# Kernel optimization log

Measured on AMD Instinct MI355X. Metric: run time of the kernel, lower is better.

The kernel has to match this reference:

```python
import jax, jax.numpy as jnp
import numpy as np

B, NA, LAT, HID, AF, L = 512, 58, 64, 128, 10, 2
N = B * NA
E = N * 16


def silu(x):
    return x * jax.nn.sigmoid(x)


def setup_inputs() -> dict:
    key = jax.random.key(0)
    ks = list(jax.random.split(key, 32))

    def p(k, shape, fan_in):
        return jax.random.normal(k, shape, jnp.float32) / np.sqrt(fan_in)

    inp = {
        "z": jax.random.normal(ks[0], (B, LAT), jnp.float32),
        "atom_types": jax.random.uniform(ks[1], (N, AF), jnp.float32),
        "edge_index": jax.random.randint(ks[2], (2, E), 0, N, jnp.int64),
        "init_coords": jax.random.normal(ks[3], (NA, 3), jnp.float32) * 0.1,
        "latent_w": p(ks[4], (LAT, HID), LAT), "latent_b": jnp.zeros((HID,), jnp.float32),
        "atom_w": p(ks[5], (AF, HID), AF), "atom_b": jnp.zeros((HID,), jnp.float32),
        # per-layer stacked params (leading dim = num_layers)
        "edge_w1": p(ks[6], (L, 2 * HID + 1, HID), 2 * HID + 1), "edge_b1": jnp.zeros((L, HID), jnp.float32),
        "edge_w2": p(ks[7], (L, HID, HID), HID), "edge_b2": jnp.zeros((L, HID), jnp.float32),
        "node_w1": p(ks[8], (L, 2 * HID, HID), 2 * HID), "node_b1": jnp.zeros((L, HID), jnp.float32),
        "node_w2": p(ks[9], (L, HID, HID), HID), "node_b2": jnp.zeros((L, HID), jnp.float32),
        "coord_w1": p(ks[10], (L, HID, HID), HID), "coord_b1": jnp.zeros((L, HID), jnp.float32),
        "coord_w2": p(ks[11], (L, HID, 1), HID),  # no bias
        "ln_g": jnp.ones((L, HID), jnp.float32), "ln_b": jnp.zeros((L, HID), jnp.float32),
        "head_w1": p(ks[12], (HID, HID // 2), HID), "head_b1": jnp.zeros((HID // 2,), jnp.float32),
        "head_w2": p(ks[13], (HID // 2, 3), HID // 2), "head_b2": jnp.zeros((3,), jnp.float32),
    }
    return inp


def _layer(h, pos, row, col, ew1, eb1, ew2, eb2, nw1, nb1, nw2, nb2, cw1, cb1, cw2, lg, lb):
    n = h.shape[0]
    xi, xj = h[row], h[col]                      # [E,HID] gathers
    rel = pos[row] - pos[col]                    # [E,3]
    d2 = jnp.clip(jnp.sum(rel * rel, axis=-1, keepdims=True), 1e-6, 1e6)
    ef = jnp.concatenate([xi, xj, d2], axis=-1)  # [E,2H+1]
    m = silu(silu(ef @ ew1 + eb1) @ ew2 + eb2)   # edge MLP messages [E,HID]
    agg = jax.ops.segment_sum(m, row, num_segments=n)
    hn = silu(jnp.concatenate([h, agg], axis=-1) @ nw1 + nb1) @ nw2 + nb2
    mu = jnp.mean(hn, axis=-1, keepdims=True)
    var = jnp.mean((hn - mu) ** 2, axis=-1, keepdims=True)
    hn = (hn - mu) * jax.lax.rsqrt(var + 1e-5) * lg + lb
    cw = jnp.clip(silu(m @ cw1 + cb1) @ cw2, -1.0, 1.0)  # [E,1]
    upd = jax.ops.segment_sum(cw * rel, row, num_segments=n)  # [N,3]
    deg = jax.ops.segment_sum(jnp.ones((row.shape[0],), pos.dtype), row, num_segments=n)[:, None]
    pos_new = pos + upd / (deg + 1e-6)
    return hn, pos_new


def reference(z, atom_types, edge_index, init_coords, latent_w, latent_b, atom_w, atom_b,
              edge_w1, edge_b1, edge_w2, edge_b2, node_w1, node_b1, node_w2, node_b2,
              coord_w1, coord_b1, coord_w2, ln_g, ln_b, head_w1, head_b1, head_w2, head_b2):
    b = z.shape[0]
    na = init_coords.shape[0]
    n = b * na
    h = z @ latent_w + latent_b                              # [B,HID]
    h = jnp.broadcast_to(h[:, None, :], (b, na, h.shape[-1])).reshape(n, -1)
    h = h + (atom_types @ atom_w + atom_b)
    pos = jnp.broadcast_to(init_coords[None], (b, na, 3)).reshape(n, 3)
    row, col = edge_index[0], edge_index[1]
    for l in range(edge_w1.shape[0]):
        h, pos = _layer(h, pos, row, col,
                        edge_w1[l], edge_b1[l], edge_w2[l], edge_b2[l],
                        node_w1[l], node_b1[l], node_w2[l], node_b2[l],
                        coord_w1[l], coord_b1[l], coord_w2[l], ln_g[l], ln_b[l])
    delta = silu(h @ head_w1 + head_b1) @ head_w2 + head_b2
    return pos + delta
```

## Files before the change

### kernel.cpp

```cpp
#include <hip/hip_runtime.h>
#include <hip/hip_bf16.h>

#define BB 512
#define NA 58
#define LAT 64
#define HID 128
#define AF 10
#define NL 2
#define NN (BB*NA)
#define NE (NN*16)
#define ET 64
#define NTILE (NE/ET)
#define PBLK 768

typedef __attribute__((ext_vector_type(8))) short s8;
typedef __attribute__((ext_vector_type(4))) float f4;

struct CvtDesc {
    const void* src[24];
    float*      dst[24];
    int         len[24];
};

struct PackJobs {
    const float* src[11];
    short*       dst[11];
    int          K[11];
    int          mode[11];
};

__device__ __forceinline__ float siluf(float x) {
    return x * __builtin_amdgcn_rcpf(1.0f + __expf(-x));
}

__device__ __forceinline__ short f2b(float x) {
    __hip_bfloat16 b = __float2bfloat16(x);
    return *(short*)&b;
}

__device__ __forceinline__ float b2f(short s) {
    return __uint_as_float(((unsigned int)(unsigned short)s) << 16);
}

__global__ void k_detect(const unsigned short* __restrict__ z16,
                         const unsigned int* __restrict__ e32,
                         int* __restrict__ flags) {
    __shared__ int sbf, si64;
    if (threadIdx.x == 0) { sbf = 0; si64 = 0; }
    __syncthreads();
    int c1 = 0, c2 = 0;
    for (int i = threadIdx.x; i < 1024; i += 256) {
        unsigned short v = z16[2*i];
        int e = (v >> 7) & 0xFF;
        if (e >= 100 && e <= 140) c1++;
        if (e32[2*i + 1] == 0u) c2++;
    }
    atomicAdd(&sbf, c1);
    atomicAdd(&si64, c2);
    __syncthreads();
    if (threadIdx.x == 0) {
        flags[0] = (sbf  > 600) ? 1 : 0;
        flags[1] = (si64 > 600) ? 1 : 0;
    }
}

__global__ void k_convert(CvtDesc d, const int* __restrict__ flags) {
    int a = blockIdx.y;
    int i = blockIdx.x * blockDim.x + threadIdx.x;
    int n = d.len[a];
    if (i >= n) return;
    if (flags[0]) {
        d.dst[a][i] = __bfloat162float(((const __hip_bfloat16*)d.src[a])[i]);
    } else {
        d.dst[a][i] = ((const float*)d.src[a])[i];
    }
}

__global__ void k_packall(PackJobs pj) {
    int j = blockIdx.y;
    int idx = blockIdx.x * 256 + threadIdx.x;
    const float* w = pj.src[j];
    short* o = pj.dst[j];
    int mode = pj.mode[j];
    if (mode == 0) {
        int K = pj.K[j];
        if (idx >= 128*K) return;
        int jj = idx & 7;
        int l  = (idx >> 3) & 63;
        int rest = idx >> 9;
        int KC = K >> 5;
        int kc = rest % KC;
        int nt = rest / KC;
        int n = nt*16 + (l & 15);
        int k = kc*32 + (l >> 4)*8 + jj;
        o[idx] = f2b(w[k*128 + n]);
    } else if (mode == 1) {
        if (idx >= 32768) return;
        int jj = idx & 7;
        int l  = (idx >> 3) & 63;
        int rest = idx >> 9;
        int kc = rest & 3;
        int nt = rest >> 2;
        int n = nt*16 + (l & 15);
        int k = kc*32 + (l >> 4)*8 + jj;
        float v = (n < 128) ? w[k*128 + n] : w[(128 + k)*128 + (n - 128)];
        o[idx] = f2b(v);
    } else {
        if (idx >= 8192) return;
        int jj = idx & 7;
        int l  = (idx >> 3) & 63;
        int rest = idx >> 9;
        int kc = rest & 3;
        int nt = rest >> 2;
        int n = nt*16 + (l & 15);
        int k = kc*32 + (l >> 4)*8 + jj;
        o[idx] = f2b(w[k*64 + n]);
    }
}

__global__ void k_hist(const int* __restrict__ eidx, const int* __restrict__ flags,
                       int* __restrict__ cnt) {
    int e = blockIdx.x * 256 + threadIdx.x;
    if (e >= NE) return;
    int is64 = flags[1];
    int r = eidx[is64 ? 2*(long)e : (long)e];
    atomicAdd(&cnt[r], 1);
}

__global__ __launch_bounds__(1024) void k_scan(const int* __restrict__ cnt,
                                               int* __restrict__ rowStart,
                                               int* __restrict__ cursor) {
    __shared__ int part[1024];
    int t = threadIdx.x;
    int base = t * 29;
    int loc[29];
    int s = 0;
    #pragma unroll
    for (int i = 0; i < 29; ++i) { loc[i] = s; s += cnt[base + i]; }
    part[t] = s;
    __syncthreads();
    for (int d = 1; d < 1024; d <<= 1) {
        int v = (t >= d) ? part[t - d] : 0;
        __syncthreads();
        part[t] += v;
        __syncthreads();
    }
    int pre = (t == 0) ? 0 : part[t - 1];
    #pragma unroll
    for (int i = 0; i < 29; ++i) {
        int v = pre + loc[i];
        rowStart[base + i] = v;
        cursor[base + i] = v;
    }
    if (t == 1023) rowStart[NN] = pre + s;
}

__global__ void k_scatter(const int* __restrict__ eidx, const int* __restrict__ flags,
                          int* __restrict__ cursor,
                          int* __restrict__ rS, int* __restrict__ cS) {
    int e = blockIdx.x * 256 + threadIdx.x;
    if (e >= NE) return;
    int is64 = flags[1];
    long ge = e, gc = (long)e + NE;
    int r = eidx[is64 ? 2*ge : ge];
    int c = eidx[is64 ? 2*gc : gc];
    int p = atomicAdd(&cursor[r], 1);
    rS[p] = r; cS[p] = c;
}

__global__ __launch_bounds__(256) void k_init3(
    const float* __restrict__ z, const float* __restrict__ lw,
    const float* __restrict__ lbz,
    const float* __restrict__ at,
    const float* __restrict__ aw, const float* __restrict__ ab,
    const float* __restrict__ ic,
    float* __restrict__ pos, short* __restrict__ hb,
    const short* __restrict__ wcat0, const float* __restrict__ b10,
    short* __restrict__ H1, float* __restrict__ agg, float* __restrict__ upd)
{
    __shared__ short x[64][136];
    __shared__ float awS[AF][HID];
    __shared__ float atS[64][AF+2];
    __shared__ float zbS[3][LAT];
    __shared__ float hzS[3][HID];
    const int tid = threadIdx.x;
    const int n0 = blockIdx.x * 64;
    const int b0 = n0 / NA;
    const int nb = (n0 + 63) / NA - b0 + 1;

    for (int i = tid; i < AF*HID; i += 256) awS[i/HID][i%HID] = aw[i];
    for (int i = tid; i < 64*AF; i += 256)
        atS[i/AF][i%AF] = at[(long)(n0 + i/AF)*AF + i%AF];
    for (int i = tid; i < nb*LAT; i += 256) {
        int bi = i / LAT, k = i - bi*LAT;
        int bidx = b0 + bi;
        zbS[bi][k] = (bidx < BB) ? z[bidx*LAT + k] : 0.f;
    }
    __syncthreads();

    for (int i = tid; i < nb*HID; i += 256) {
        int bi = i / HID, c = i - bi*HID;
        float acc = lbz[c];
        #pragma unroll
        for (int k = 0; k < LAT; ++k) acc += zbS[bi][k] * lw[k*HID + c];
        hzS[bi][c] = acc;
    }
    __syncthreads();

    #pragma unroll
    for (int it = 0; it < 32; ++it) {
        int idx = it*256 + tid;
        int r = idx >> 7, c = idx & 127;
        int n = n0 + r;
        float v = hzS[n/NA - b0][c] + ab[c];
        #pragma unroll
        for (int f = 0; f < AF; ++f) v += atS[r][f]*awS[f][c];
        short s = f2b(v);
        x[r][c] = s;
        hb[(long)n*HID + c] = s;
    }
    if (tid < 192) {
        int i = tid/3, d = tid - i*3;
        int n = n0 + i;
        pos[n*3 + d] = ic[(n % NA)*3 + d];
        upd[n*3 + d] = 0.f;
    }
    {
        f4* a4 = (f4*)(agg + (long)n0*HID);
        for (int j = tid; j < 64*HID/4; j += 256) a4[j] = (f4)0.f;
    }
    __syncthreads();

    const int l = tid & 63, w = tid >> 6;
    const int l16 = l & 15, quad = l >> 4;
    f4 acc[4][4];
    #pragma unroll
    for (int mt = 0; mt < 4; ++mt)
        #pragma unroll
        for (int nt4 = 0; nt4 < 4; ++nt4) acc[mt][nt4] = (f4)0.f;
    #pragma unroll
    for (int kc = 0; kc < 4; ++kc) {
        s8 a[4];
        #pragma unroll
        for (int mt = 0; mt < 4; ++mt)
            a[mt] = *(const s8*)&x[mt*16 + l16][kc*32 + quad*8];
        #pragma unroll
        for (int nt4 = 0; nt4 < 4; ++nt4) {
            int nt = w*4 + nt4;
            s8 b = *(const s8*)(wcat0 + (((size_t)nt*4 + kc)*64 + l)*8);
            #pragma unroll
            for (int mt = 0; mt < 4; ++mt)
                acc[mt][nt4] = __builtin_amdgcn_mfma_f32_16x16x32_bf16(a[mt], b, acc[mt][nt4], 0, 0, 0);
        }
    }
    #pragma unroll
    for (int nt4 = 0; nt4 < 4; ++nt4) {
        int col = (w*4 + nt4)*16 + l16;
        float bias = (col < 128) ? b10[col] : 0.f;
        #pragma unroll
        for (int mt = 0; mt < 4; ++mt)
            #pragma unroll
            for (int i = 0; i < 4; ++i) {
                int row = mt*16 + quad*4 + i;
                H1[(long)(n0 + row)*256 + col] = f2b(acc[mt][nt4][i] + bias);
            }
    }
}

__global__ __launch_bounds__(256, 3) void k_edge8(
    const short* __restrict__ H1,
    const int* __restrict__ rS, const int* __restrict__ cS,
    const float* __restrict__ pos,
    const float* __restrict__ w1c,
    const short* __restrict__ w2p, const float* __restrict__ b2,
    const short* __restrict__ c1p, const float* __restrict__ cb1,
    const float* __restrict__ cw2,
    float* __restrict__ agg, float* __restrict__ upd)
{
    __shared__ short t1[2][ET][136];
    __shared__ short mm[ET][136];
    __shared__ int   rIs[2][ET], cIs[2][ET];
    __shared__ float sred[ET];

    const int tid = threadIdx.x;
    const int l = tid & 63, w = tid >> 6;
    const int l16 = l & 15, quad = l >> 4;
    const int c0 = (2*w)*16 + l16, c1c = (2*w+1)*16 + l16;
    const int half = tid >> 7, ch = tid & 127;
    const int q = tid & 15;
    const int esub = tid >> 4;

    float wv[8];
    #pragma unroll
    for (int j = 0; j < 8; ++j) wv[j] = w1c[q*8 + j];

    s8 w2f[8], c1f[8];
    #pragma unroll
    for (int kc = 0; kc < 4; ++kc) {
        w2f[kc]     = *(const s8*)(w2p + (((size_t)(2*w)*4 + kc)*64 + l)*8);
        w2f[4 + kc] = *(const s8*)(w2p + (((size_t)(2*w+1)*4 + kc)*64 + l)*8);
        c1f[kc]     = *(const s8*)(c1p + (((size_t)(2*w)*4 + kc)*64 + l)*8);
        c1f[4 + kc] = *(const s8*)(c1p + (((size_t)(2*w+1)*4 + kc)*64 + l)*8);
    }
    const float bia2_0 = b2[c0],  bia2_1 = b2[c1c];
    const float biac_0 = cb1[c0], biac_1 = cb1[c1c];
    const float cw0    = cw2[c0], cw1v   = cw2[c1c];

    int   pri[4], pci[4];
    float pd2[4];
    auto PREIDX = [&](int T) {
        long eb = (long)T * ET;
        #pragma unroll
        for (int it = 0; it < 4; ++it) {
            int e = esub + 16*it;
            int r = rS[eb + e], c = cS[eb + e];
            pri[it] = r; pci[it] = c;
            float rx = pos[r*3+0] - pos[c*3+0];
            float ry = pos[r*3+1] - pos[c*3+1];
            float rz = pos[r*3+2] - pos[c*3+2];
            pd2[it] = fminf(fmaxf(rx*rx + ry*ry + rz*rz, 1e-6f), 1e6f);
        }
    };

    int T = blockIdx.x;
    PREIDX(T);
    #pragma unroll
    for (int it = 0; it < 4; ++it) {
        s8 va = *(const s8*)(H1 + (long)pri[it]*256 + q*8);
        s8 vb = *(const s8*)(H1 + (long)pci[it]*256 + 128 + q*8);
        float d2 = pd2[it];
        s8 o;
        #pragma unroll
        for (int j = 0; j < 8; ++j)
            o[j] = f2b(siluf(b2f(va[j]) + b2f(vb[j]) + d2*wv[j]));
        *(s8*)&t1[0][esub + 16*it][q*8] = o;
    }
    if (q == 0) {
        #pragma unroll
        for (int it = 0; it < 4; ++it) {
            rIs[0][esub + 16*it] = pri[it];
            cIs[0][esub + 16*it] = pci[it];
        }
    }
    if (tid < ET) sred[tid] = 0.f;
    int Tn = T + PBLK;
    if (Tn < NTILE) PREIDX(Tn);
    __syncthreads();

    int b = 0;
    while (true) {
        const bool hasNext = (Tn < NTILE);

        {
            f4 acc[4][2];
            #pragma unroll
            for (int mt = 0; mt < 4; ++mt) { acc[mt][0] = (f4)0.f; acc[mt][1] = (f4)0.f; }
            #pragma unroll
            for (int it = 0; it < 4; ++it) {
                s8 va, vb;
                if (hasNext) {
                    va = *(const s8*)(H1 + (long)pri[it]*256 + q*8);
                    vb = *(const s8*)(H1 + (long)pci[it]*256 + 128 + q*8);
                }
                #pragma unroll
                for (int mt = 0; mt < 4; ++mt) {
                    s8 a = *(const s8*)&t1[b][mt*16 + l16][it*32 + quad*8];
                    acc[mt][0] = __builtin_amdgcn_mfma_f32_16x16x32_bf16(a, w2f[it],     acc[mt][0], 0, 0, 0);
                    acc[mt][1] = __builtin_amdgcn_mfma_f32_16x16x32_bf16(a, w2f[4 + it], acc[mt][1], 0, 0, 0);
                }
                if (hasNext) {
                    float d2 = pd2[it];
                    s8 o;
                    #pragma unroll
                    for (int j = 0; j < 8; ++j)
                        o[j] = f2b(siluf(b2f(va[j]) + b2f(vb[j]) + d2*wv[j]));
                    *(s8*)&t1[b^1][esub + 16*it][q*8] = o;
                }
            }
            if (hasNext && q == 0) {
                #pragma unroll
                for (int it = 0; it < 4; ++it) {
                    rIs[b^1][esub + 16*it] = pri[it];
                    cIs[b^1][esub + 16*it] = pci[it];
                }
            }
            #pragma unroll
            for (int mt = 0; mt < 4; ++mt) {
                #pragma unroll
                for (int i = 0; i < 4; ++i) {
                    int row = mt*16 + quad*4 + i;
                    mm[row][c0]  = f2b(siluf(acc[mt][0][i] + bia2_0));
                    mm[row][c1c] = f2b(siluf(acc[mt][1][i] + bia2_1));
                }
            }
        }
        __syncthreads();

        {
            int e0 = half * 32;
            int cur = rIs[b][e0];
            float a = 0.f;
            #pragma unroll
            for (int e = e0; e < e0 + 32; ++e) {
                int r = rIs[b][e];
                if (r != cur) {
                    atomicAdd(&agg[(long)cur*HID + ch], a);
                    a = 0.f; cur = r;
                }
                a += b2f(mm[e][ch]);
            }
            atomicAdd(&agg[(long)cur*HID + ch], a);
        }
        {
            f4 acc[4][2];
            #pragma unroll
            for (int mt = 0; mt < 4; ++mt) { acc[mt][0] = (f4)0.f; acc[mt][1] = (f4)0.f; }
            #pragma unroll
            for (int kc = 0; kc < 4; ++kc) {
                #pragma unroll
                for (int mt = 0; mt < 4; ++mt) {
                    s8 a = *(const s8*)&mm[mt*16 + l16][kc*32 + quad*8];
                    acc[mt][0] = __builtin_amdgcn_mfma_f32_16x16x32_bf16(a, c1f[kc],     acc[mt][0], 0, 0, 0);
                    acc[mt][1] = __builtin_amdgcn_mfma_f32_16x16x32_bf16(a, c1f[4 + kc], acc[mt][1], 0, 0, 0);
                }
            }
            #pragma unroll
            for (int mt = 0; mt < 4; ++mt) {
                #pragma unroll
                for (int i = 0; i < 4; ++i) {
                    float p = siluf(acc[mt][0][i] + biac_0) * cw0
                            + siluf(acc[mt][1][i] + biac_1) * cw1v;
                    p += __shfl_xor(p, 1);
                    p += __shfl_xor(p, 2);
                    p += __shfl_xor(p, 4);
                    p += __shfl_xor(p, 8);
                    if (l16 == 0) {
                        int row = mt*16 + quad*4 + i;
                        atomicAdd(&sred[row], p);
                    }
                }
            }
        }
        int Tnn = Tn + PBLK;
        if (hasNext && Tnn < NTILE) PREIDX(Tnn);
        __syncthreads();

        if (tid < ET) {
            float cwv = fminf(fmaxf(sred[tid], -1.f), 1.f);
            sred[tid] = 0.f;
            int r = rIs[b][tid], c = cIs[b][tid];
            float rx = pos[r*3+0] - pos[c*3+0];
            float ry = pos[r*3+1] - pos[c*3+1];
            float rz = pos[r*3+2] - pos[c*3+2];
            atomicAdd(&upd[r*3+0], cwv*rx);
            atomicAdd(&upd[r*3+1], cwv*ry);
            atomicAdd(&upd[r*3+2], cwv*rz);
        }
        if (!hasNext) break;
        T = Tn; Tn = Tnn; b ^= 1;
    }
}

__global__ __launch_bounds__(256) void k_node_mfma(
    short* __restrict__ hb, float* __restrict__ agg,
    const short* __restrict__ w1p, const float* __restrict__ b1n,
    const short* __restrict__ w2p, const float* __restrict__ b2n,
    const float* __restrict__ lg, const float* __restrict__ lb,
    float* __restrict__ pos, float* __restrict__ upd,
    const int* __restrict__ rowStart,
    const short* __restrict__ wcatn, const float* __restrict__ b1next,
    short* __restrict__ H1,
    const short* __restrict__ hw1p, const float* __restrict__ hb1,
    const float* __restrict__ hw2, const float* __restrict__ hb2,
    void* __restrict__ out, const int* __restrict__ flags)
{
    __shared__ short x[64][264];
    __shared__ short t1[64][144];
    __shared__ float mus[64], rstds[64];
    __shared__ float posS[64][3];
    float (*hn)[132] = (float (*)[132])&x[0][0];
    float (*hid)[68] = (float (*)[68])&x[0][0];

    const int tid = threadIdx.x;
    const int n0 = blockIdx.x * 64;

    #pragma unroll
    for (int it = 0; it < 4; ++it) {
        int idx = it*256 + tid;
        int e = idx >> 4, qq = idx & 15;
        *(int4*)&x[e][qq*8] = *(const int4*)(hb + (long)(n0+e)*HID + qq*8);
    }
    #pragma unroll
    for (int it = 0; it < 8; ++it) {
        int idx = it*256 + tid;
        int e = idx >> 5, qq = idx & 31;
        float4 v = *(const float4*)(agg + (long)(n0+e)*HID + qq*4);
        short4 sv;
        sv.x = f2b(v.x); sv.y = f2b(v.y); sv.z = f2b(v.z); sv.w = f2b(v.w);
        *(short4*)&x[e][128 + qq*4] = sv;
    }
    __syncthreads();

    {
        f4* a4 = (f4*)(agg + (long)n0*HID);
        for (int j = tid; j < 64*HID/4; j += 256) a4[j] = (f4)0.f;
    }

    const int l = tid & 63, w = tid >> 6;
    const int l16 = l & 15, quad = l >> 4;
    const int nt0 = 2*w, nt1 = 2*w + 1;
    const int c0 = nt0*16 + l16, c1c = nt1*16 + l16;

    {
        f4 acc[4][2];
        #pragma unroll
        for (int mt = 0; mt < 4; ++mt) { acc[mt][0] = (f4)0.f; acc[mt][1] = (f4)0.f; }
        #pragma unroll
        for (int kc = 0; kc < 8; ++kc) {
            s8 b0  = *(const s8*)(w1p + (((size_t)nt0*8 + kc)*64 + l)*8);
            s8 b1f = *(const s8*)(w1p + (((size_t)nt1*8 + kc)*64 + l)*8);
            #pragma unroll
            for (int mt = 0; mt < 4; ++mt) {
                s8 a = *(const s8*)&x[mt*16 + l16][kc*32 + quad*8];
                acc[mt][0] = __builtin_amdgcn_mfma_f32_16x16x32_bf16(a, b0,  acc[mt][0], 0, 0, 0);
                acc[mt][1] = __builtin_amdgcn_mfma_f32_16x16x32_bf16(a, b1f, acc[mt][1], 0, 0, 0);
            }
        }
        float bia0 = b1n[c0], bia1 = b1n[c1c];
        #pragma unroll
        for (int mt = 0; mt < 4; ++mt) {
            #pragma unroll
            for (int i = 0; i < 4; ++i) {
                int row = mt*16 + quad*4 + i;
                t1[row][c0]  = f2b(siluf(acc[mt][0][i] + bia0));
                t1[row][c1c] = f2b(siluf(acc[mt][1][i] + bia1));
            }
        }
    }
    __syncthreads();

    {
        f4 acc[4][2];
        #pragma unroll
        for (int mt = 0; mt < 4; ++mt) { acc[mt][0] = (f4)0.f; acc[mt][1] = (f4)0.f; }
        #pragma unroll
        for (int kc = 0; kc < 4; ++kc) {
            s8 b0  = *(const s8*)(w2p + (((size_t)nt0*4 + kc)*64 + l)*8);
            s8 b1f = *(const s8*)(w2p + (((size_t)nt1*4 + kc)*64 + l)*8);
            #pragma unroll
            for (int mt = 0; mt < 4; ++mt) {
                s8 a = *(const s8*)&t1[mt*16 + l16][kc*32 + quad*8];
                acc[mt][0] = __builtin_amdgcn_mfma_f32_16x16x32_bf16(a, b0,  acc[mt][0], 0, 0, 0);
                acc[mt][1] = __builtin_amdgcn_mfma_f32_16x16x32_bf16(a, b1f, acc[mt][1], 0, 0, 0);
            }
        }
        float bia0 = b2n[c0], bia1 = b2n[c1c];
        __syncthreads();
        #pragma unroll
        for (int mt = 0; mt < 4; ++mt) {
            #pragma unroll
            for (int i = 0; i < 4; ++i) {
                int row = mt*16 + quad*4 + i;
                hn[row][c0]  = acc[mt][0][i] + bia0;
                hn[row][c1c] = acc[mt][1][i] + bia1;
            }
        }
    }
    __syncthreads();

    {
        int r = tid >> 2, part = tid & 3;
        float s = 0.f, qv = 0.f;
        #pragma unroll
        for (int j = 0; j < 32; ++j) {
            float v = hn[r][part + 4*j];
            s += v; qv += v*v;
        }
        s += __shfl_xor(s, 1); qv += __shfl_xor(qv, 1);
        s += __shfl_xor(s, 2); qv += __shfl_xor(qv, 2);
        if (part == 0) {
            float mu = s * (1.0f/HID);
            float var = qv * (1.0f/HID) - mu*mu;
            mus[r] = mu;
            rstds[r] = rsqrtf(var + 1e-5f);
        }
    }
    __syncthreads();

    #pragma unroll
    for (int it = 0; it < 32; ++it) {
        int idx = it*256 + tid;
        int r = idx >> 7, c = idx & 127;
        float v = (hn[r][c] - mus[r]) * rstds[r] * lg[c] + lb[c];
        short s = f2b(v);
        hb[(long)(n0 + r)*HID + c] = s;
        t1[r][c] = s;
    }
    if (tid < 192) {
        int i = tid / 3, d = tid - i*3;
        int n = n0 + i;
        float dg = (float)(rowStart[n+1] - rowStart[n]);
        float np = pos[n*3+d] + upd[n*3+d] / (dg + 1e-6f);
        pos[n*3+d] = np;
        posS[i][d] = np;
        upd[n*3+d] = 0.f;
    }
    __syncthreads();

    if (wcatn) {
        f4 acc[4][4];
        #pragma unroll
        for (int mt = 0; mt < 4; ++mt)
            #pragma unroll
            for (int nt4 = 0; nt4 < 4; ++nt4) acc[mt][nt4] = (f4)0.f;
        #pragma unroll
        for (int kc = 0; kc < 4; ++kc) {
            s8 a[4];
            #pragma unroll
            for (int mt = 0; mt < 4; ++mt)
                a[mt] = *(const s8*)&t1[mt*16 + l16][kc*32 + quad*8];
            #pragma unroll
            for (int nt4 = 0; nt4 < 4; ++nt4) {
                int nt = w*4 + nt4;
                s8 b = *(const s8*)(wcatn + (((size_t)nt*4 + kc)*64 + l)*8);
                #pragma unroll
                for (int mt = 0; mt < 4; ++mt)
                    acc[mt][nt4] = __builtin_amdgcn_mfma_f32_16x16x32_bf16(a[mt], b, acc[mt][nt4], 0, 0, 0);
            }
        }
        #pragma unroll
        for (int nt4 = 0; nt4 < 4; ++nt4) {
            int col = (w*4 + nt4)*16 + l16;
            float bias = (col < 128) ? b1next[col] : 0.f;
            #pragma unroll
            for (int mt = 0; mt < 4; ++mt)
                #pragma unroll
                for (int i = 0; i < 4; ++i) {
                    int row = mt*16 + quad*4 + i;
                    H1[(long)(n0 + row)*256 + col] = f2b(acc[mt][nt4][i] + bias);
                }
        }
    } else {
        f4 acc[4];
        #pragma unroll
        for (int mt = 0; mt < 4; ++mt) acc[mt] = (f4)0.f;
        #pragma unroll
        for (int kc = 0; kc < 4; ++kc) {
            s8 b = *(const s8*)(hw1p + (((size_t)w*4 + kc)*64 + l)*8);
            #pragma unroll
            for (int mt = 0; mt < 4; ++mt) {
                s8 a = *(const s8*)&t1[mt*16 + l16][kc*32 + quad*8];
                acc[mt] = __builtin_amdgcn_mfma_f32_16x16x32_bf16(a, b, acc[mt], 0, 0, 0);
            }
        }
        int col = w*16 + l16;
        float bias = hb1[col];
        #pragma unroll
        for (int mt = 0; mt < 4; ++mt)
            #pragma unroll
            for (int i = 0; i < 4; ++i) {
                int row = mt*16 + quad*4 + i;
                hid[row][col] = siluf(acc[mt][i] + bias);
            }
        __syncthreads();
        if (tid < 192) {
            int r = tid / 3, cc = tid - r*3;
            float a2 = hb2[cc];
            #pragma unroll
            for (int k = 0; k < 64; ++k) a2 += hid[r][k] * hw2[k*3 + cc];
            int n = n0 + r;
            float v = posS[r][cc] + a2;
            if (flags[0]) ((__hip_bfloat16*)out)[n*3+cc] = __float2bfloat16(v);
            else          ((float*)out)[n*3+cc] = v;
        }
    }
}

extern "C" void kernel_launch(void* const* d_in, const int* in_sizes, int n_in,
                              void* d_out, int out_size, void* d_ws, size_t ws_size,
                              hipStream_t stream)
{
    (void)in_sizes; (void)n_in; (void)out_size; (void)ws_size;

    int* flags = (int*)d_ws;
    float* base = (float*)d_ws;
    size_t off = 64;
    auto alloc = [&](size_t n) { float* p = base + off; off += (n + 63) & ~63ull; return p; };

    static const int aidx[24] = {0,1,3,4,5,6,7,8,9,10,11,12,13,14,15,16,17,18,19,20,21,22,23,24};
    static const int alen[24] = {
        BB*LAT, NN*AF, NA*3, LAT*HID, HID, AF*HID, HID,
        NL*257*HID, NL*HID, NL*HID*HID, NL*HID,
        NL*256*HID, NL*HID, NL*HID*HID, NL*HID,
        NL*HID*HID, NL*HID, NL*HID, NL*HID, NL*HID,
        HID*64, 64, 64*3, 3
    };
    CvtDesc cd;
    float* fp[24];
    for (int a = 0; a < 24; ++a) {
        fp[a] = alloc((size_t)alen[a]);
        cd.src[a] = d_in[aidx[a]];
        cd.dst[a] = fp[a];
        cd.len[a] = alen[a];
    }
    float* agg = alloc((size_t)NN*HID);
    float* pos = alloc((size_t)NN*3);
    float* upd = alloc((size_t)NN*3);
    short* hb  = (short*)alloc((size_t)NN*HID/2);
    short* H1  = (short*)alloc((size_t)NN*256/2);
    short* wcatp = (short*)alloc((size_t)NL*32768/2);
    short* w2p = (short*)alloc((size_t)NL*16384/2);
    short* c1p = (short*)alloc((size_t)NL*16384/2);
    short* nw1p = (short*)alloc((size_t)NL*32768/2);
    short* nw2p = (short*)alloc((size_t)NL*16384/2);
    short* hw1p = (short*)alloc((size_t)8192/2);
    int* cnt      = (int*)alloc((size_t)NN);
    int* rowStart = (int*)alloc((size_t)NN + 1);
    int* cursor   = (int*)alloc((size_t)NN);
    int* rS       = (int*)alloc((size_t)NE);
    int* cS       = (int*)alloc((size_t)NE);
    const int* eidx = (const int*)d_in[2];

    k_detect<<<1, 256, 0, stream>>>((const unsigned short*)d_in[0],
                                    (const unsigned int*)d_in[2], flags);
    k_convert<<<dim3((NN*AF + 255)/256, 24), 256, 0, stream>>>(cd, flags);

    PackJobs pj;
    for (int l = 0; l < NL; ++l) {
        int b5 = l*5;
        pj.src[b5+0] = fp[7]  + (size_t)l*257*HID; pj.dst[b5+0] = wcatp + (size_t)l*32768; pj.K[b5+0] = 256; pj.mode[b5+0] = 1;
        pj.src[b5+1] = fp[9]  + (size_t)l*HID*HID; pj.dst[b5+1] = w2p   + (size_t)l*16384; pj.K[b5+1] = 128; pj.mode[b5+1] = 0;
        pj.src[b5+2] = fp[15] + (size_t)l*HID*HID; pj.dst[b5+2] = c1p   + (size_t)l*16384; pj.K[b5+2] = 128; pj.mode[b5+2] = 0;
        pj.src[b5+3] = fp[11] + (size_t)l*256*HID; pj.dst[b5+3] = nw1p  + (size_t)l*32768; pj.K[b5+3] = 256; pj.mode[b5+3] = 0;
        pj.src[b5+4] = fp[13] + (size_t)l*HID*HID; pj.dst[b5+4] = nw2p  + (size_t)l*16384; pj.K[b5+4] = 128; pj.mode[b5+4] = 0;
    }
    pj.src[10] = fp[20]; pj.dst[10] = hw1p; pj.K[10] = 128; pj.mode[10] = 2;
    k_packall<<<dim3(128, 11), 256, 0, stream>>>(pj);

    hipMemsetAsync(cnt, 0, (size_t)NN*sizeof(int), stream);
    k_hist<<<(NE + 255)/256, 256, 0, stream>>>(eidx, flags, cnt);
    k_scan<<<1, 1024, 0, stream>>>(cnt, rowStart, cursor);
    k_scatter<<<(NE + 255)/256, 256, 0, stream>>>(eidx, flags, cursor, rS, cS);

    k_init3<<<NN/64, 256, 0, stream>>>(fp[0], fp[3], fp[4],
                                       fp[1], fp[5], fp[6], fp[2], pos, hb,
                                       wcatp, fp[8], H1, agg, upd);

    for (int l = 0; l < NL; ++l) {
        k_edge8<<<PBLK, 256, 0, stream>>>(H1, rS, cS, pos,
            fp[7] + (size_t)l*257*HID + 256*HID,
            w2p + (size_t)l*16384, fp[10] + (size_t)l*HID,
            c1p + (size_t)l*16384, fp[16] + (size_t)l*HID,
            fp[17] + (size_t)l*HID,
            agg, upd);
        const short* wcatn = (l+1 < NL) ? (wcatp + (size_t)(l+1)*32768) : nullptr;
        const float* b1nx  = (l+1 < NL) ? (fp[8] + (size_t)(l+1)*HID) : fp[8];
        k_node_mfma<<<NN/64, 256, 0, stream>>>(hb, agg,
            nw1p + (size_t)l*32768, fp[12] + (size_t)l*HID,
            nw2p + (size_t)l*16384, fp[14] + (size_t)l*HID,
            fp[18] + (size_t)l*HID, fp[19] + (size_t)l*HID,
            pos, upd, rowStart, wcatn, b1nx, H1,
            hw1p, fp[21], fp[22], fp[23], d_out, flags);
    }
}
```

Measured before the change: 597.6 us.

## Alias edge message buffer onto consumed t1 slot to raise edge-kernel occupancy

Removes the separate mm shared-memory buffer by writing edge messages into the current t1 slot once the second GEMM has consumed it. This needs an extra block barrier. Cutting LDS use lets the launch bound go from 3 to 4 blocks per CU, and the persistent grid grows from 768 to 1024 blocks to match. The position-difference loads for the coordinate update are also moved ahead of the barrier to hide their latency. The risks are the extra sync per tile and register pressure from the tighter launch bound.

After: 738.4 us. 1.24x slower.

```diff
diff --git a/kernel.cpp b/kernel.cpp
--- a/kernel.cpp
+++ b/kernel.cpp
@@ -11,7 +11,7 @@
 #define NE (NN*16)
 #define ET 64
 #define NTILE (NE/ET)
-#define PBLK 768
+#define PBLK 1024
 
 typedef __attribute__((ext_vector_type(8))) short s8;
 typedef __attribute__((ext_vector_type(4))) float f4;
@@ -267,7 +267,7 @@
     }
 }
 
-__global__ __launch_bounds__(256, 3) void k_edge8(
+__global__ __launch_bounds__(256, 4) void k_edge8(
     const short* __restrict__ H1,
     const int* __restrict__ rS, const int* __restrict__ cS,
     const float* __restrict__ pos,
@@ -278,7 +278,6 @@
     float* __restrict__ agg, float* __restrict__ upd)
 {
     __shared__ short t1[2][ET][136];
-    __shared__ short mm[ET][136];
     __shared__ int   rIs[2][ET], cIs[2][ET];
     __shared__ float sred[ET];
 
@@ -351,8 +350,8 @@
     while (true) {
         const bool hasNext = (Tn < NTILE);
 
+        f4 acc[4][2];
         {
-            f4 acc[4][2];
             #pragma unroll
             for (int mt = 0; mt < 4; ++mt) { acc[mt][0] = (f4)0.f; acc[mt][1] = (f4)0.f; }
             #pragma unroll
@@ -384,14 +383,17 @@
                     cIs[b^1][esub + 16*it] = pci[it];
                 }
             }
-            #pragma unroll
-            for (int mt = 0; mt < 4; ++mt) {
-                #pragma unroll
-                for (int i = 0; i < 4; ++i) {
-                    int row = mt*16 + quad*4 + i;
-                    mm[row][c0]  = f2b(siluf(acc[mt][0][i] + bia2_0));
-                    mm[row][c1c] = f2b(siluf(acc[mt][1][i] + bia2_1));
-                }
+        }
+        __syncthreads();
+
+        short (*mm)[136] = t1[b];
+        #pragma unroll
+        for (int mt = 0; mt < 4; ++mt) {
+            #pragma unroll
+            for (int i = 0; i < 4; ++i) {
+                int row = mt*16 + quad*4 + i;
+                mm[row][c0]  = f2b(siluf(acc[mt][0][i] + bia2_0));
+                mm[row][c1c] = f2b(siluf(acc[mt][1][i] + bia2_1));
             }
         }
         __syncthreads();
@@ -412,24 +414,24 @@
             atomicAdd(&agg[(long)cur*HID + ch], a);
         }
         {
-            f4 acc[4][2];
-            #pragma unroll
-            for (int mt = 0; mt < 4; ++mt) { acc[mt][0] = (f4)0.f; acc[mt][1] = (f4)0.f; }
+            f4 acc3[4][2];
+            #pragma unroll
+            for (int mt = 0; mt < 4; ++mt) { acc3[mt][0] = (f4)0.f; acc3[mt][1] = (f4)0.f; }
             #pragma unroll
             for (int kc = 0; kc < 4; ++kc) {
                 #pragma unroll
                 for (int mt = 0; mt < 4; ++mt) {
                     s8 a = *(const s8*)&mm[mt*16 + l16][kc*32 + quad*8];
-                    acc[mt][0] = __builtin_amdgcn_mfma_f32_16x16x32_bf16(a, c1f[kc],     acc[mt][0], 0, 0, 0);
-                    acc[mt][1] = __builtin_amdgcn_mfma_f32_16x16x32_bf16(a, c1f[4 + kc], acc[mt][1], 0, 0, 0);
+                    acc3[mt][0] = __builtin_amdgcn_mfma_f32_16x16x32_bf16(a, c1f[kc],     acc3[mt][0], 0, 0, 0);
+                    acc3[mt][1] = __builtin_amdgcn_mfma_f32_16x16x32_bf16(a, c1f[4 + kc], acc3[mt][1], 0, 0, 0);
                 }
             }
             #pragma unroll
             for (int mt = 0; mt < 4; ++mt) {
                 #pragma unroll
                 for (int i = 0; i < 4; ++i) {
-                    float p = siluf(acc[mt][0][i] + biac_0) * cw0
-                            + siluf(acc[mt][1][i] + biac_1) * cw1v;
+                    float p = siluf(acc3[mt][0][i] + biac_0) * cw0
+                            + siluf(acc3[mt][1][i] + biac_1) * cw1v;
                     p += __shfl_xor(p, 1);
                     p += __shfl_xor(p, 2);
                     p += __shfl_xor(p, 4);
@@ -441,6 +443,15 @@
                 }
             }
         }
+        int   ur = 0;
+        float urx = 0.f, ury = 0.f, urz = 0.f;
+        if (tid < ET) {
+            ur = rIs[b][tid];
+            int uc = cIs[b][tid];
+            urx = pos[ur*3+0] - pos[uc*3+0];
+            ury = pos[ur*3+1] - pos[uc*3+1];
+            urz = pos[ur*3+2] - pos[uc*3+2];
+        }
         int Tnn = Tn + PBLK;
         if (hasNext && Tnn < NTILE) PREIDX(Tnn);
         __syncthreads();
@@ -448,13 +459,9 @@
         if (tid < ET) {
             float cwv = fminf(fmaxf(sred[tid], -1.f), 1.f);
             sred[tid] = 0.f;
-            int r = rIs[b][tid], c = cIs[b][tid];
-            float rx = pos[r*3+0] - pos[c*3+0];
-            float ry = pos[r*3+1] - pos[c*3+1];
-            float rz = pos[r*3+2] - pos[c*3+2];
-            atomicAdd(&upd[r*3+0], cwv*rx);
-            atomicAdd(&upd[r*3+1], cwv*ry);
-            atomicAdd(&upd[r*3+2], cwv*rz);
+            atomicAdd(&upd[ur*3+0], cwv*urx);
+            atomicAdd(&upd[ur*3+1], cwv*ury);
+            atomicAdd(&upd[ur*3+2], cwv*urz);
         }
         if (!hasNext) break;
         T = Tn; Tn = Tnn; b ^= 1;
```
